# Kernel optimization log

Measured on AMD Instinct MI355X. Metric: run time of the kernel, lower is better.

Reference implementation:

```python
import jax, jax.numpy as jnp
import numpy as np
from jax import lax

DIM = 256
MOTION = 128
HEADS = 8
HID = int(DIM * 3.0)
EPS = 1e-5


def std_ln(x, w, b):
    # standard nn.LayerNorm: biased var, /sqrt(var+eps)
    mean = x.mean(-1, keepdims=True)
    var = jnp.var(x, axis=-1, keepdims=True)
    return w * (x - mean) / jnp.sqrt(var + EPS) + b


def custom_ln(x, w, b):
    # repo's custom LayerNorm: UNBIASED std (ddof=1) and divide by (std+eps)
    mean = x.mean(-1, keepdims=True)
    std = jnp.std(x, axis=-1, ddof=1, keepdims=True)
    return w * (x - mean) / (std + EPS) + b


def setup_inputs() -> dict:
    key = jax.random.key(0)
    ks = jax.random.split(key, 32)
    s = 0.02
    d = {}
    d['x'] = jax.random.normal(ks[0], (4, 16384, DIM), jnp.float32)
    d['cor'] = jax.random.uniform(ks[1], (4, 128, 128, 2), jnp.float32)
    # attention projections (qkv_bias=False)
    d['q_w'] = jax.random.normal(ks[2], (DIM, DIM), jnp.float32) * s
    d['kv_w'] = jax.random.normal(ks[3], (2 * DIM, DIM), jnp.float32) * s
    d['cor_w'] = jax.random.normal(ks[4], (MOTION, 2), jnp.float32) * s
    hd = DIM // HEADS
    md = MOTION // HEADS
    d['kln_w'] = jnp.ones((HEADS, 1, hd), jnp.float32)
    d['kln_b'] = jnp.zeros((HEADS, 1, hd), jnp.float32)
    d['vln_w'] = jnp.ones((HEADS, 1, hd), jnp.float32)
    d['vln_b'] = jnp.zeros((HEADS, 1, hd), jnp.float32)
    d['corln_w'] = jnp.ones((HEADS, 1, md), jnp.float32)
    d['corln_b'] = jnp.zeros((HEADS, 1, md), jnp.float32)
    d['op1_w'] = jax.random.normal(ks[5], (DIM, DIM), jnp.float32) * s
    d['op1_b'] = jnp.zeros((DIM,), jnp.float32)
    d['op2_w'] = jax.random.normal(ks[6], (DIM, DIM), jnp.float32) * s
    d['op2_b'] = jnp.zeros((DIM,), jnp.float32)
    d['om1_w'] = jax.random.normal(ks[7], (MOTION, MOTION), jnp.float32) * s
    d['om1_b'] = jnp.zeros((MOTION,), jnp.float32)
    d['om2_w'] = jax.random.normal(ks[8], (MOTION, MOTION), jnp.float32) * s
    d['om2_b'] = jnp.zeros((MOTION,), jnp.float32)
    d['norm1_w'] = jnp.ones((DIM,), jnp.float32)
    d['norm1_b'] = jnp.zeros((DIM,), jnp.float32)
    d['norm2_w'] = jnp.ones((DIM,), jnp.float32)
    d['norm2_b'] = jnp.zeros((DIM,), jnp.float32)
    d['fc1_w'] = jax.random.normal(ks[9], (HID, DIM), jnp.float32) * s
    d['fc1_b'] = jnp.zeros((HID,), jnp.float32)
    d['dw_w'] = jax.random.normal(ks[10], (HID, 1, 3, 3), jnp.float32) * np.sqrt(2.0 / 9.0)
    d['dw_b'] = jnp.zeros((HID,), jnp.float32)
    d['fc2_w'] = jax.random.normal(ks[11], (DIM, HID), jnp.float32) * s
    d['fc2_b'] = jnp.zeros((DIM,), jnp.float32)
    d['H'] = 128
    d['W'] = 128
    d['B'] = 2
    return d


def _forward(x, cor, q_w, kv_w, cor_w, kln_w, kln_b, vln_w, vln_b,
             corln_w, corln_b, op1_w, op1_b, op2_w, op2_b,
             om1_w, om1_b, om2_w, om2_b, norm1_w, norm1_b,
             norm2_w, norm2_b, fc1_w, fc1_b, dw_w, dw_b, fc2_w, fc2_b,
             H, W, B):
    gelu = lambda t: jax.nn.gelu(t, approximate=False)
    nwB = 2 * B
    N = H * W
    C = x.shape[-1]
    M = cor_w.shape[0]
    h = kln_w.shape[0]
    hd = C // h
    md = M // h
    hid = fc1_w.shape[0]

    xw = x.reshape(nwB, N, C)            # window_partition with full window == identity
    corw = cor.reshape(nwB, N, 2)

    xn = std_ln(xw, norm1_w, norm1_b)
    half = nwB // 2
    xr = jnp.concatenate([xn[half:], xn[:half]], axis=0)  # swap frame halves

    q = (xn @ q_w.T).reshape(nwB, N, h, hd).transpose(0, 2, 1, 3)          # bhnd
    kv = (xr @ kv_w.T).reshape(nwB, N, 2, h, hd)
    k = kv[:, :, 0].transpose(0, 2, 1, 3)
    v = kv[:, :, 1].transpose(0, 2, 1, 3)
    ce_flat = corw @ cor_w.T                                               # (nwB,N,M)
    ce = ce_flat.reshape(nwB, N, h, md).transpose(0, 2, 1, 3)

    k = custom_ln(k, kln_w, kln_b)
    v = custom_ln(v, vln_w, vln_b)
    ce = custom_ln(ce, corln_w, corln_b)

    # linear attention: (k^T v)/N then q @ .
    ktv = jnp.einsum('bhnd,bhne->bhde', k, v) / N
    app = jnp.einsum('bhnd,bhde->bhne', q, ktv).transpose(0, 2, 1, 3).reshape(nwB, N, C)
    t = app + xn                                   # shortcut bias = x_norm
    x_app = gelu(t @ op1_w.T + op1_b) @ op2_w.T + op2_b + xn

    ktc = jnp.einsum('bhnd,bhne->bhde', k, ce) / N
    crev = jnp.einsum('bhnd,bhde->bhne', q, ktc).transpose(0, 2, 1, 3).reshape(nwB, N, M)
    dm = crev - ce_flat
    motion = gelu(dm @ om1_w.T + om1_b) @ om2_w.T + om2_b

    x_back = xn + x_app

    # Mlp with depthwise conv
    y = std_ln(x_back, norm2_w, norm2_b)
    h1 = y @ fc1_w.T + fc1_b                       # (nwB,N,hid)
    img = h1.transpose(0, 2, 1).reshape(nwB, hid, H, W)
    conv = lax.conv_general_dilated(img, dw_w, (1, 1), 'SAME',
                                    feature_group_count=hid,
                                    dimension_numbers=('NCHW', 'OIHW', 'NCHW'))
    conv = conv + dw_b[None, :, None, None]
    h2 = gelu(conv.reshape(nwB, hid, N).transpose(0, 2, 1))
    out = h2 @ fc2_w.T + fc2_b

    x_out = xw + out
    return x_out, motion


def reference(x, cor, q_w, kv_w, cor_w, kln_w, kln_b, vln_w, vln_b,
              corln_w, corln_b, op1_w, op1_b, op2_w, op2_b,
              om1_w, om1_b, om2_w, om2_b, norm1_w, norm1_b,
              norm2_w, norm2_b, fc1_w, fc1_b, dw_w, dw_b, fc2_w, fc2_b,
              H, W, B):
    return _forward(x, cor, q_w, kv_w, cor_w, kln_w, kln_b, vln_w, vln_b,
                    corln_w, corln_b, op1_w, op1_b, op2_w, op2_b,
                    om1_w, om1_b, om2_w, om2_b, norm1_w, norm1_b,
                    norm2_w, norm2_b, fc1_w, fc1_b, dw_w, dw_b, fc2_w, fc2_b,
                    H, W, B)
```

## Files before the change

### kernel.cpp

```cpp
#include <hip/hip_runtime.h>
#include <hip/hip_bf16.h>

#define NTOK 65536

typedef __attribute__((ext_vector_type(4))) float f32x4;
typedef __attribute__((ext_vector_type(8))) short bf16x8;

__device__ __forceinline__ float gelu_f(float x){
    float z = -2.30234438f * fmaf(0.044715f * x * x, x, x);
    float e = exp2f(z);
    return x * __builtin_amdgcn_rcpf(1.0f + e);
}
__device__ __forceinline__ float bf2f(unsigned short u){
    union { unsigned int i; float f; } w; w.i = ((unsigned int)u) << 16; return w.f;
}
__device__ __forceinline__ unsigned short f2bf(float f){
    __hip_bfloat16 h = __float2bfloat16(f);
    return *reinterpret_cast<unsigned short*>(&h);
}

__global__ __launch_bounds__(256) void wconv_kernel(const float* __restrict__ q_w, const float* __restrict__ kv_w,
                                                    const float* __restrict__ op1_w, const float* __restrict__ op2_w,
                                                    const float* __restrict__ om1_w, const float* __restrict__ om2_w,
                                                    const float* __restrict__ fc1_w, const float* __restrict__ fc2_w,
                                                    unsigned short* __restrict__ Wb){
    size_t e = ((size_t)blockIdx.x * 256 + threadIdx.x) * 4;
    if (e >= 753664) return;
    const float* src; size_t off;
    if      (e <  65536){ src = q_w;   off = 0; }
    else if (e < 196608){ src = kv_w;  off = 65536; }
    else if (e < 262144){ src = op1_w; off = 196608; }
    else if (e < 327680){ src = op2_w; off = 262144; }
    else if (e < 344064){ src = om1_w; off = 327680; }
    else if (e < 360448){ src = om2_w; off = 344064; }
    else if (e < 557056){ src = fc1_w; off = 360448; }
    else                { src = fc2_w; off = 557056; }
    float4 v = *reinterpret_cast<const float4*>(src + (e - off));
    ushort4 o; o.x = f2bf(v.x); o.y = f2bf(v.y); o.z = f2bf(v.z); o.w = f2bf(v.w);
    *reinterpret_cast<ushort4*>(Wb + e) = o;
}

template<bool BF16IN>
__global__ __launch_bounds__(256) void stdln_kernel(const void* __restrict__ Xp,
                                                    const float* __restrict__ w,
                                                    const float* __restrict__ b,
                                                    unsigned short* __restrict__ out){
    int wv = threadIdx.x >> 6, lane = threadIdx.x & 63;
    int tok0 = (blockIdx.x * 4 + wv) * 8;
    int c0 = lane * 4;
    float4 w4 = *reinterpret_cast<const float4*>(w + c0);
    float4 b4 = *reinterpret_cast<const float4*>(b + c0);
    #pragma unroll 2
    for (int j = 0; j < 8; j++){
        size_t base = (size_t)(tok0 + j) * 256 + c0;
        float v[4];
        if constexpr (BF16IN){
            ushort4 u = *reinterpret_cast<const ushort4*>((const unsigned short*)Xp + base);
            v[0] = bf2f(u.x); v[1] = bf2f(u.y); v[2] = bf2f(u.z); v[3] = bf2f(u.w);
        } else {
            float4 f = *reinterpret_cast<const float4*>((const float*)Xp + base);
            v[0] = f.x; v[1] = f.y; v[2] = f.z; v[3] = f.w;
        }
        float s = v[0] + v[1] + v[2] + v[3];
        #pragma unroll
        for (int m = 1; m < 64; m <<= 1) s += __shfl_xor(s, m, 64);
        float mean = s * (1.0f / 256.0f);
        float ss = 0;
        #pragma unroll
        for (int k = 0; k < 4; k++){ v[k] -= mean; ss = fmaf(v[k], v[k], ss); }
        #pragma unroll
        for (int m = 1; m < 64; m <<= 1) ss += __shfl_xor(ss, m, 64);
        float inv = rsqrtf(ss * (1.0f / 256.0f) + 1e-5f);
        ushort4 o;
        o.x = f2bf(w4.x * v[0] * inv + b4.x);
        o.y = f2bf(w4.y * v[1] * inv + b4.y);
        o.z = f2bf(w4.z * v[2] * inv + b4.z);
        o.w = f2bf(w4.w * v[3] * inv + b4.w);
        *reinterpret_cast<ushort4*>(out + base) = o;
    }
}

__global__ __launch_bounds__(256) void ce_kernel(const float* __restrict__ cor,
                                                 const float* __restrict__ cor_w,
                                                 unsigned short* __restrict__ CEF){
    int m = threadIdx.x & 127, half = threadIdx.x >> 7;
    float w0 = cor_w[m * 2 + 0], w1 = cor_w[m * 2 + 1];
    #pragma unroll 4
    for (int it = 0; it < 16; it++){
        int tok = blockIdx.x * 32 + it * 2 + half;
        float c0 = cor[(size_t)tok * 2 + 0];
        float c1 = cor[(size_t)tok * 2 + 1];
        CEF[(size_t)tok * 128 + m] = f2bf(c0 * w0 + c1 * w1);
    }
}

__global__ __launch_bounds__(256) void ktvc_kernel(const unsigned short* __restrict__ Kb,
                                                   const unsigned short* __restrict__ Vb,
                                                   const unsigned short* __restrict__ CEF,
                                                   const float* __restrict__ kw, const float* __restrict__ kbb,
                                                   const float* __restrict__ vw, const float* __restrict__ vbb,
                                                   const float* __restrict__ cw, const float* __restrict__ cbb,
                                                   float* __restrict__ KTV, float* __restrict__ KTC){
    int bh = blockIdx.x, b = bh >> 3, h = bh & 7;
    __shared__ float Ks[64][36];
    __shared__ float Vs[64][36];
    __shared__ float Cs[64][20];
    __shared__ float P[2][64][24];
    int t = threadIdx.x;
    int lr = t >> 2, lq = t & 3;
    int g = t >> 6, tl = t & 63;
    int d0 = (tl >> 3) * 4, e0 = (tl & 7) * 4, e0c = (tl & 7) * 2;
    float kwr[8], kbr[8], vwr[8], vbr[8], cwr[4], cbr[4];
    #pragma unroll
    for (int j = 0; j < 8; j++){
        kwr[j] = kw[h * 32 + lq * 8 + j]; kbr[j] = kbb[h * 32 + lq * 8 + j];
        vwr[j] = vw[h * 32 + lq * 8 + j]; vbr[j] = vbb[h * 32 + lq * 8 + j];
    }
    #pragma unroll
    for (int j = 0; j < 4; j++){
        cwr[j] = cw[h * 16 + lq * 4 + j]; cbr[j] = cbb[h * 16 + lq * 4 + j];
    }
    float akv[4][4] = {};
    float akc[4][2] = {};
    size_t base = ((size_t)b << 14) + (size_t)blockIdx.y * 512;
    for (int n0 = 0; n0 < 512; n0 += 64){
        size_t rowi = base + n0 + lr;
        const ushort4* kp = reinterpret_cast<const ushort4*>(Kb + rowi * 256 + h * 32 + lq * 8);
        ushort4 ka = kp[0], kc = kp[1];
        const ushort4* vp = reinterpret_cast<const ushort4*>(Vb + rowi * 256 + h * 32 + lq * 8);
        ushort4 va = vp[0], vc = vp[1];
        ushort4 ca = *reinterpret_cast<const ushort4*>(CEF + rowi * 128 + h * 16 + lq * 4);
        float kvv[8] = { bf2f(ka.x), bf2f(ka.y), bf2f(ka.z), bf2f(ka.w),
                         bf2f(kc.x), bf2f(kc.y), bf2f(kc.z), bf2f(kc.w) };
        float vvv[8] = { bf2f(va.x), bf2f(va.y), bf2f(va.z), bf2f(va.w),
                         bf2f(vc.x), bf2f(vc.y), bf2f(vc.z), bf2f(vc.w) };
        float cvv[4] = { bf2f(ca.x), bf2f(ca.y), bf2f(ca.z), bf2f(ca.w) };
        float s = 0;
        #pragma unroll
        for (int j = 0; j < 8; j++) s += kvv[j];
        s += __shfl_xor(s, 1, 64); s += __shfl_xor(s, 2, 64);
        float mean = s * (1.0f / 32.0f);
        float ss = 0;
        #pragma unroll
        for (int j = 0; j < 8; j++){ kvv[j] -= mean; ss = fmaf(kvv[j], kvv[j], ss); }
        ss += __shfl_xor(ss, 1, 64); ss += __shfl_xor(ss, 2, 64);
        float inv = 1.0f / (sqrtf(ss * (1.0f / 31.0f)) + 1e-5f);
        #pragma unroll
        for (int j = 0; j < 8; j++) kvv[j] = fmaf(kwr[j] * kvv[j], inv, kbr[j]);
        s = 0;
        #pragma unroll
        for (int j = 0; j < 8; j++) s += vvv[j];
        s += __shfl_xor(s, 1, 64); s += __shfl_xor(s, 2, 64);
        mean = s * (1.0f / 32.0f);
        ss = 0;
        #pragma unroll
        for (int j = 0; j < 8; j++){ vvv[j] -= mean; ss = fmaf(vvv[j], vvv[j], ss); }
        ss += __shfl_xor(ss, 1, 64); ss += __shfl_xor(ss, 2, 64);
        inv = 1.0f / (sqrtf(ss * (1.0f / 31.0f)) + 1e-5f);
        #pragma unroll
        for (int j = 0; j < 8; j++) vvv[j] = fmaf(vwr[j] * vvv[j], inv, vbr[j]);
        s = 0;
        #pragma unroll
        for (int j = 0; j < 4; j++) s += cvv[j];
        s += __shfl_xor(s, 1, 64); s += __shfl_xor(s, 2, 64);
        mean = s * (1.0f / 16.0f);
        ss = 0;
        #pragma unroll
        for (int j = 0; j < 4; j++){ cvv[j] -= mean; ss = fmaf(cvv[j], cvv[j], ss); }
        ss += __shfl_xor(ss, 1, 64); ss += __shfl_xor(ss, 2, 64);
        inv = 1.0f / (sqrtf(ss * (1.0f / 15.0f)) + 1e-5f);
        #pragma unroll
        for (int j = 0; j < 4; j++) cvv[j] = fmaf(cwr[j] * cvv[j], inv, cbr[j]);
        __syncthreads();
        #pragma unroll
        for (int j = 0; j < 8; j++){ Ks[lr][lq * 8 + j] = kvv[j]; Vs[lr][lq * 8 + j] = vvv[j]; }
        #pragma unroll
        for (int j = 0; j < 4; j++) Cs[lr][lq * 4 + j] = cvv[j];
        __syncthreads();
        #pragma unroll 4
        for (int i = 0; i < 16; i++){
            int n = g * 16 + i;
            float4 k4 = *reinterpret_cast<const float4*>(&Ks[n][d0]);
            float4 v4 = *reinterpret_cast<const float4*>(&Vs[n][e0]);
            float2 c2 = *reinterpret_cast<const float2*>(&Cs[n][e0c]);
            float kk[4] = { k4.x, k4.y, k4.z, k4.w };
            float vv[4] = { v4.x, v4.y, v4.z, v4.w };
            #pragma unroll
            for (int a = 0; a < 4; a++){
                akv[a][0] = fmaf(kk[a], vv[0], akv[a][0]);
                akv[a][1] = fmaf(kk[a], vv[1], akv[a][1]);
                akv[a][2] = fmaf(kk[a], vv[2], akv[a][2]);
                akv[a][3] = fmaf(kk[a], vv[3], akv[a][3]);
                akc[a][0] = fmaf(kk[a], c2.x, akc[a][0]);
                akc[a][1] = fmaf(kk[a], c2.y, akc[a][1]);
            }
        }
    }
    __syncthreads();
    if (g >= 2){
        float* p = &P[g - 2][tl][0];
        #pragma unroll
        for (int a = 0; a < 4; a++){
            #pragma unroll
            for (int e = 0; e < 4; e++) p[a * 4 + e] = akv[a][e];
            p[16 + a * 2 + 0] = akc[a][0];
            p[16 + a * 2 + 1] = akc[a][1];
        }
    }
    __syncthreads();
    if (g < 2){
        const float* p = &P[g][tl][0];
        #pragma unroll
        for (int a = 0; a < 4; a++){
            #pragma unroll
            for (int e = 0; e < 4; e++) akv[a][e] += p[a * 4 + e];
            akc[a][0] += p[16 + a * 2 + 0];
            akc[a][1] += p[16 + a * 2 + 1];
        }
    }
    __syncthreads();
    if (g == 1){
        float* p = &P[0][tl][0];
        #pragma unroll
        for (int a = 0; a < 4; a++){
            #pragma unroll
            for (int e = 0; e < 4; e++) p[a * 4 + e] = akv[a][e];
            p[16 + a * 2 + 0] = akc[a][0];
            p[16 + a * 2 + 1] = akc[a][1];
        }
    }
    __syncthreads();
    if (g == 0){
        const float* p = &P[0][tl][0];
        const float sc = 1.0f / 16384.0f;
        float* o = KTV + (size_t)bh * 1024;
        float* o2 = KTC + (size_t)bh * 512;
        #pragma unroll
        for (int a = 0; a < 4; a++){
            #pragma unroll
            for (int e = 0; e < 4; e++)
                atomicAdd(&o[(d0 + a) * 32 + e0 + e], (akv[a][e] + p[a * 4 + e]) * sc);
            atomicAdd(&o2[(d0 + a) * 16 + e0c + 0], (akc[a][0] + p[16 + a * 2 + 0]) * sc);
            atomicAdd(&o2[(d0 + a) * 16 + e0c + 1], (akc[a][1] + p[16 + a * 2 + 1]) * sc);
        }
    }
}

__global__ __launch_bounds__(256) void wcomb_kernel(const float* __restrict__ q_w,
                                                    const float* __restrict__ KTV,
                                                    const float* __restrict__ KTC,
                                                    unsigned short* __restrict__ WTC){
    int c = blockIdx.x;
    int b = blockIdx.y;
    int i = threadIdx.x;
    __shared__ float coef[32];
    int h = (c < 256) ? (c >> 5) : ((c - 256) >> 4);
    if (i < 32){
        if (c < 256) coef[i] = KTV[(size_t)((b * 8 + h) << 10) + i * 32 + (c & 31)];
        else         coef[i] = KTC[(size_t)((b * 8 + h) << 9)  + i * 16 + ((c - 256) & 15)];
    }
    __syncthreads();
    float acc = 0;
    #pragma unroll
    for (int d = 0; d < 32; d++) acc = fmaf(q_w[(size_t)(h * 32 + d) * 256 + i], coef[d], acc);
    WTC[((size_t)b * 384 + c) * 256 + i] = f2bf(acc);
}

__global__ __launch_bounds__(192) void dwconv_kernel(const unsigned short* __restrict__ H1,
                                                     const float* __restrict__ dww,
                                                     const float* __restrict__ dwb,
                                                     unsigned short* __restrict__ H2){
    int blk = blockIdx.x;
    int xq = blk & 3;
    int yb = (blk >> 2) & 31;
    int bb = blk >> 7;
    int y0 = yb * 4, x0 = xq * 32;
    int ch = threadIdx.x * 4;
    float w[9][4];
    #pragma unroll
    for (int k = 0; k < 9; k++)
        #pragma unroll
        for (int j = 0; j < 4; j++) w[k][j] = dww[(ch + j) * 9 + k];
    float bias[4] = { dwb[ch], dwb[ch+1], dwb[ch+2], dwb[ch+3] };
    size_t rb[6]; bool rv[6];
    #pragma unroll
    for (int r = 0; r < 6; r++){
        int yr = y0 - 1 + r;
        rv[r] = ((unsigned)yr <= 127u);
        int yc = yr < 0 ? 0 : (yr > 127 ? 127 : yr);
        rb[r] = ((size_t)((bb << 14) + (yc << 7))) * 768 + ch;
    }
    size_t ob[4];
    #pragma unroll
    for (int j = 0; j < 4; j++) ob[j] = ((size_t)((bb << 14) + ((y0 + j) << 7))) * 768 + ch;

    ushort4 cA[6], cB[6], cC[6], cD[6];
    const ushort4 Z = {0, 0, 0, 0};
    #define LOADR(DST, XX) do {                                               \
        int _x = (XX);                                                        \
        bool xv = ((unsigned)_x <= 127u);                                     \
        _Pragma("unroll")                                                     \
        for (int r = 0; r < 6; r++)                                           \
            DST[r] = (xv && rv[r]) ? *reinterpret_cast<const ushort4*>(H1 + rb[r] + (size_t)_x * 768) : Z; \
    } while (0)

    #define EMITB(SA, SB, SC, XX) do {                                        \
        _Pragma("unroll")                                                     \
        for (int j = 0; j < 4; j++){                                          \
            float acc[4];                                                     \
            _Pragma("unroll")                                                 \
            for (int q = 0; q < 4; q++) acc[q] = bias[q];                     \
            _Pragma("unroll")                                                 \
            for (int rr2 = 0; rr2 < 3; rr2++){                                \
                int ri = j + rr2;                                             \
                float a0=bf2f(SA[ri].x),a1=bf2f(SA[ri].y),a2=bf2f(SA[ri].z),a3=bf2f(SA[ri].w); \
                float b0=bf2f(SB[ri].x),b1=bf2f(SB[ri].y),b2=bf2f(SB[ri].z),b3=bf2f(SB[ri].w); \
                float c0=bf2f(SC[ri].x),c1=bf2f(SC[ri].y),c2=bf2f(SC[ri].z),c3=bf2f(SC[ri].w); \
                acc[0]=fmaf(a0,w[rr2*3+0][0],acc[0]); acc[0]=fmaf(b0,w[rr2*3+1][0],acc[0]); acc[0]=fmaf(c0,w[rr2*3+2][0],acc[0]); \
                acc[1]=fmaf(a1,w[rr2*3+0][1],acc[1]); acc[1]=fmaf(b1,w[rr2*3+1][1],acc[1]); acc[1]=fmaf(c1,w[rr2*3+2][1],acc[1]); \
                acc[2]=fmaf(a2,w[rr2*3+0][2],acc[2]); acc[2]=fmaf(b2,w[rr2*3+1][2],acc[2]); acc[2]=fmaf(c2,w[rr2*3+2][2],acc[2]); \
                acc[3]=fmaf(a3,w[rr2*3+0][3],acc[3]); acc[3]=fmaf(b3,w[rr2*3+1][3],acc[3]); acc[3]=fmaf(c3,w[rr2*3+2][3],acc[3]); \
            }                                                                 \
            ushort4 o;                                                        \
            o.x = f2bf(gelu_f(acc[0])); o.y = f2bf(gelu_f(acc[1]));           \
            o.z = f2bf(gelu_f(acc[2])); o.w = f2bf(gelu_f(acc[3]));           \
            *reinterpret_cast<ushort4*>(H2 + ob[j] + (size_t)(XX) * 768) = o; \
        }                                                                     \
    } while (0)

    LOADR(cD, x0 - 1);
    LOADR(cA, x0);
    LOADR(cB, x0 + 1);
    LOADR(cC, x0 + 2);
    #pragma unroll 1
    for (int g = 0; g < 8; g++){
        int x = x0 + g * 4;
        EMITB(cD, cA, cB, x);     LOADR(cD, x + 3);
        EMITB(cA, cB, cC, x + 1); LOADR(cA, x + 4);
        EMITB(cB, cC, cD, x + 2); LOADR(cB, x + 5);
        EMITB(cC, cD, cA, x + 3); LOADR(cC, x + 6);
    }
    #undef LOADR
    #undef EMITB
}

#define M_KV        1
#define M_BIAS_GELU 2
#define M_BIAS_ADD2 3
#define M_BIAS      4
#define M_BIAS_BF16 5
#define M_BIAS_ADDX 6
#define M_ATTN      7

template<int MODE, bool SWAP, int K, int O, int WN>
__global__ __launch_bounds__(128 * WN) void mgemm(const unsigned short* __restrict__ A,
                                                  const unsigned short* __restrict__ Wp,
                                                  const float* __restrict__ bias,
                                                  const void* __restrict__ add,
                                                  void* __restrict__ out0,
                                                  void* __restrict__ out1){
    constexpr int WAVES = 2 * WN;
    constexpr int BN = 64 * WN;
    constexpr int CH = 8 + 4 * WN;
    constexpr int NT = K / 32;
    __shared__ __align__(16) unsigned short As[2][128 * 32];
    __shared__ __align__(16) unsigned short Bs[2][BN * 32];
    const int t = threadIdx.x;
    const int lane = t & 63, wid = t >> 6;
    const int wm = wid & 1, wn = wid >> 1;
    const int row0 = blockIdx.x * 128;
    const int colB = blockIdx.y * BN;
    const unsigned short* W = Wp;
    if constexpr (MODE == M_ATTN) W += (size_t)(row0 >> 14) * (384 * 256);
    f32x4 acc[4][4];
    #pragma unroll
    for (int i = 0; i < 4; i++)
        #pragma unroll
        for (int j = 0; j < 4; j++){ f32x4 z = {0.f, 0.f, 0.f, 0.f}; acc[i][j] = z; }

    const int lr = lane >> 2;
    const int ls = lane & 3;
    const int kq = lane >> 4;
    const int rr = lane & 15;

    auto STAGE = [&](int buf, int kb){
        #pragma unroll
        for (int c = wid; c < CH; c += WAVES){
            int r16 = (c < 8) ? c : (c - 8);
            int row = r16 * 16 + lr;
            int ko = ls ^ ((row >> 1) & 3);
            if (c < 8){
                int ga = row0 + row;
                if (SWAP) ga ^= 32768;
                __builtin_amdgcn_global_load_lds(
                    (const __attribute__((address_space(1))) unsigned int*)(A + (size_t)ga * K + kb + ko * 8),
                    (__attribute__((address_space(3))) unsigned int*)(As[buf] + r16 * 512),
                    16, 0, 0);
            } else {
                int gc = colB + row;
                __builtin_amdgcn_global_load_lds(
                    (const __attribute__((address_space(1))) unsigned int*)(W + (size_t)gc * K + kb + ko * 8),
                    (__attribute__((address_space(3))) unsigned int*)(Bs[buf] + r16 * 512),
                    16, 0, 0);
            }
        }
    };

    STAGE(0, 0);
    asm volatile("s_waitcnt vmcnt(0)" ::: "memory");
    __builtin_amdgcn_s_barrier();
    #pragma unroll 1
    for (int tt = 0; tt < NT; tt++){
        int cur = tt & 1;
        if (tt + 1 < NT) STAGE(cur ^ 1, (tt + 1) * 32);
        bf16x8 af[4], bfr[4];
        #pragma unroll
        for (int m = 0; m < 4; m++){
            int row = wm * 64 + m * 16 + rr;
            int s = kq ^ ((row >> 1) & 3);
            af[m] = *reinterpret_cast<const bf16x8*>(As[cur] + row * 32 + s * 8);
        }
        #pragma unroll
        for (int n = 0; n < 4; n++){
            int row = wn * 64 + n * 16 + rr;
            int s = kq ^ ((row >> 1) & 3);
            bfr[n] = *reinterpret_cast<const bf16x8*>(Bs[cur] + row * 32 + s * 8);
        }
        #pragma unroll
        for (int m = 0; m < 4; m++)
            #pragma unroll
            for (int n = 0; n < 4; n++)
                acc[m][n] = __builtin_amdgcn_mfma_f32_16x16x32_bf16(af[m], bfr[n], acc[m][n], 0, 0, 0);
        if (tt + 1 < NT){
            asm volatile("s_waitcnt vmcnt(0)" ::: "memory");
            __builtin_amdgcn_s_barrier();
        }
    }

    #pragma unroll
    for (int m = 0; m < 4; m++){
        #pragma unroll
        for (int n = 0; n < 4; n++){
            int col = colB + wn * 64 + n * 16 + rr;
            int rbase = row0 + wm * 64 + m * 16 + kq * 4;
            #pragma unroll
            for (int j = 0; j < 4; j++){
                int r = rbase + j;
                float v = acc[m][n][j];
                size_t o = (size_t)r * O + col;
                if constexpr (MODE == M_KV){
                    if (col < 256) ((unsigned short*)out0)[(size_t)r * 256 + col] = f2bf(v);
                    else           ((unsigned short*)out1)[(size_t)r * 256 + col - 256] = f2bf(v);
                } else if constexpr (MODE == M_BIAS_GELU){
                    ((unsigned short*)out0)[o] = f2bf(gelu_f(v + bias[col]));
                } else if constexpr (MODE == M_BIAS_ADD2){
                    ((unsigned short*)out0)[o] = f2bf(v + bias[col] + 2.0f * bf2f(((const unsigned short*)add)[o]));
                } else if constexpr (MODE == M_BIAS){
                    ((float*)out0)[o] = v + bias[col];
                } else if constexpr (MODE == M_BIAS_BF16){
                    ((unsigned short*)out0)[o] = f2bf(v + bias[col]);
                } else if constexpr (MODE == M_BIAS_ADDX){
                    ((float*)out0)[o] = v + bias[col] + ((const float*)add)[o];
                } else if constexpr (MODE == M_ATTN){
                    if (col < 256){
                        size_t o1 = (size_t)r * 256 + col;
                        ((unsigned short*)out0)[o1] = f2bf(v + bf2f(((const unsigned short*)add)[o1]));
                    } else {
                        size_t o2 = (size_t)r * 128 + (col - 256);
                        ((unsigned short*)out1)[o2] = f2bf(v - bf2f(((const unsigned short*)bias)[o2]));
                    }
                }
            }
        }
    }
}

extern "C" void kernel_launch(void* const* d_in, const int* in_sizes, int n_in,
                              void* d_out, int out_size, void* d_ws, size_t ws_size,
                              hipStream_t stream){
    const float* x     = (const float*)d_in[0];
    const float* cor   = (const float*)d_in[1];
    const float* q_w   = (const float*)d_in[2];
    const float* kv_w  = (const float*)d_in[3];
    const float* cor_w = (const float*)d_in[4];
    const float* kln_w = (const float*)d_in[5];
    const float* kln_b = (const float*)d_in[6];
    const float* vln_w = (const float*)d_in[7];
    const float* vln_b = (const float*)d_in[8];
    const float* corln_w = (const float*)d_in[9];
    const float* corln_b = (const float*)d_in[10];
    const float* op1_w = (const float*)d_in[11];
    const float* op1_b = (const float*)d_in[12];
    const float* op2_w = (const float*)d_in[13];
    const float* op2_b = (const float*)d_in[14];
    const float* om1_w = (const float*)d_in[15];
    const float* om1_b = (const float*)d_in[16];
    const float* om2_w = (const float*)d_in[17];
    const float* om2_b = (const float*)d_in[18];
    const float* n1_w  = (const float*)d_in[19];
    const float* n1_b  = (const float*)d_in[20];
    const float* n2_w  = (const float*)d_in[21];
    const float* n2_b  = (const float*)d_in[22];
    const float* fc1_w = (const float*)d_in[23];
    const float* fc1_b = (const float*)d_in[24];
    const float* dw_w  = (const float*)d_in[25];
    const float* dw_b  = (const float*)d_in[26];
    const float* fc2_w = (const float*)d_in[27];
    const float* fc2_b = (const float*)d_in[28];

    unsigned short* XN  = (unsigned short*)d_ws;
    unsigned short* Qb  = XN  + (size_t)NTOK * 256;
    unsigned short* Kb  = Qb  + (size_t)NTOK * 256;
    unsigned short* Vb  = Kb  + (size_t)NTOK * 256;
    unsigned short* CEF = Vb  + (size_t)NTOK * 256;
    unsigned short* CE  = CEF + (size_t)NTOK * 128;
    float* KTV = (float*)(CE + (size_t)NTOK * 128);
    float* KTC = KTV + 32768;
    unsigned short* WTC = (unsigned short*)(KTC + 16384);
    unsigned short* Wb  = WTC + 4 * 384 * 256;
    unsigned short* H2  = Wb + 753664;
    unsigned short* T1 = Vb;
    unsigned short* T2 = Kb;
    unsigned short* XB = Qb;
    unsigned short* Y  = Vb;
    unsigned short* TM = CE;
    unsigned short* MH = CEF;
    unsigned short* H1 = XN;
    float* xout = (float*)d_out;
    float* mout = xout + (size_t)NTOK * 256;

    unsigned short* w_kv  = Wb + 65536;
    unsigned short* w_op1 = Wb + 196608;
    unsigned short* w_op2 = Wb + 262144;
    unsigned short* w_om1 = Wb + 327680;
    unsigned short* w_om2 = Wb + 344064;
    unsigned short* w_fc1 = Wb + 360448;
    unsigned short* w_fc2 = Wb + 557056;

    wconv_kernel<<<736, 256, 0, stream>>>(q_w, kv_w, op1_w, op2_w, om1_w, om2_w, fc1_w, fc2_w, Wb);
    stdln_kernel<false><<<2048, 256, 0, stream>>>(x, n1_w, n1_b, XN);
    mgemm<M_KV, true, 256, 512, 4><<<dim3(512, 2), 512, 0, stream>>>(XN, w_kv, nullptr, nullptr, Kb, Vb);
    ce_kernel<<<2048, 256, 0, stream>>>(cor, cor_w, CEF);
    hipMemsetAsync(KTV, 0, (32768 + 16384) * sizeof(float), stream);
    ktvc_kernel<<<dim3(32, 32), 256, 0, stream>>>(Kb, Vb, CEF, kln_w, kln_b, vln_w, vln_b,
                                                  corln_w, corln_b, KTV, KTC);
    wcomb_kernel<<<dim3(384, 4), 256, 0, stream>>>(q_w, KTV, KTC, WTC);
    mgemm<M_ATTN, false, 256, 384, 6><<<dim3(512, 1), 768, 0, stream>>>(XN, WTC, (const float*)CEF, XN, T1, TM);
    mgemm<M_BIAS_GELU, false, 256, 256, 4><<<dim3(512, 1), 512, 0, stream>>>(T1, w_op1, op1_b, nullptr, T2, nullptr);
    mgemm<M_BIAS_ADD2, false, 256, 256, 4><<<dim3(512, 1), 512, 0, stream>>>(T2, w_op2, op2_b, XN, XB, nullptr);
    mgemm<M_BIAS_GELU, false, 128, 128, 2><<<dim3(512, 1), 256, 0, stream>>>(TM, w_om1, om1_b, nullptr, MH, nullptr);
    mgemm<M_BIAS, false, 128, 128, 2><<<dim3(512, 1), 256, 0, stream>>>(MH, w_om2, om2_b, nullptr, mout, nullptr);
    stdln_kernel<true><<<2048, 256, 0, stream>>>(XB, n2_w, n2_b, Y);
    mgemm<M_BIAS_BF16, false, 256, 768, 6><<<dim3(512, 2), 768, 0, stream>>>(Y, w_fc1, fc1_b, nullptr, H1, nullptr);
    dwconv_kernel<<<512, 192, 0, stream>>>(H1, dw_w, dw_b, H2);
    mgemm<M_BIAS_ADDX, false, 768, 256, 4><<<dim3(512, 1), 512, 0, stream>>>(H2, w_fc2, fc2_b, x, xout, nullptr);
}
```

Measured before the change: 424.2 us.

## Stage GEMM epilogue through LDS for vectorized coalesced stores; widen KV GEMM tile

The GEMM epilogue now writes each wave's accumulator fragment into a padded LDS scratch region and reads it back row-wise. Global loads and stores then happen in 16-byte vectors, including the residual and add operands, instead of scattered 2- or 4-byte scalar accesses. The KV projection GEMM launches with WN=8 (1024 threads, one block column) so each block covers all 512 output columns. The cost is an extra LDS round trip and a barrier per block. The rounding order of the bf16 adds changes slightly, since the GEMM result is rounded to bf16 before the residual is added.

```diff
diff --git a/kernel.cpp b/kernel.cpp
--- a/kernel.cpp
+++ b/kernel.cpp
@@ -17,6 +17,13 @@
 __device__ __forceinline__ unsigned short f2bf(float f){
     __hip_bfloat16 h = __float2bfloat16(f);
     return *reinterpret_cast<unsigned short*>(&h);
+}
+__device__ __forceinline__ bf16x8 add_bf8(bf16x8 s, bf16x8 o, float k){
+    bf16x8 r;
+    #pragma unroll
+    for (int i = 0; i < 8; i++)
+        r[i] = (short)f2bf(fmaf(k, bf2f((unsigned short)o[i]), bf2f((unsigned short)s[i])));
+    return r;
 }
 
 __global__ __launch_bounds__(256) void wconv_kernel(const float* __restrict__ q_w, const float* __restrict__ kv_w,
@@ -363,8 +370,10 @@
     constexpr int BN = 64 * WN;
     constexpr int CH = 8 + 4 * WN;
     constexpr int NT = K / 32;
-    __shared__ __align__(16) unsigned short As[2][128 * 32];
-    __shared__ __align__(16) unsigned short Bs[2][BN * 32];
+    constexpr bool F32OUT = (MODE == M_BIAS || MODE == M_BIAS_ADDX);
+    __shared__ __align__(16) unsigned short SMEM[2 * 128 * 32 + 2 * BN * 32];
+    unsigned short* As0 = SMEM;
+    unsigned short* Bs0 = SMEM + 2 * 128 * 32;
     const int t = threadIdx.x;
     const int lane = t & 63, wid = t >> 6;
     const int wm = wid & 1, wn = wid >> 1;
@@ -394,13 +403,13 @@
                 if (SWAP) ga ^= 32768;
                 __builtin_amdgcn_global_load_lds(
                     (const __attribute__((address_space(1))) unsigned int*)(A + (size_t)ga * K + kb + ko * 8),
-                    (__attribute__((address_space(3))) unsigned int*)(As[buf] + r16 * 512),
+                    (__attribute__((address_space(3))) unsigned int*)(As0 + buf * 4096 + r16 * 512),
                     16, 0, 0);
             } else {
                 int gc = colB + row;
                 __builtin_amdgcn_global_load_lds(
                     (const __attribute__((address_space(1))) unsigned int*)(W + (size_t)gc * K + kb + ko * 8),
-                    (__attribute__((address_space(3))) unsigned int*)(Bs[buf] + r16 * 512),
+                    (__attribute__((address_space(3))) unsigned int*)(Bs0 + buf * (BN * 32) + r16 * 512),
                     16, 0, 0);
             }
         }
@@ -418,13 +427,13 @@
         for (int m = 0; m < 4; m++){
             int row = wm * 64 + m * 16 + rr;
             int s = kq ^ ((row >> 1) & 3);
-            af[m] = *reinterpret_cast<const bf16x8*>(As[cur] + row * 32 + s * 8);
+            af[m] = *reinterpret_cast<const bf16x8*>(As0 + cur * 4096 + row * 32 + s * 8);
         }
         #pragma unroll
         for (int n = 0; n < 4; n++){
             int row = wn * 64 + n * 16 + rr;
             int s = kq ^ ((row >> 1) & 3);
-            bfr[n] = *reinterpret_cast<const bf16x8*>(Bs[cur] + row * 32 + s * 8);
+            bfr[n] = *reinterpret_cast<const bf16x8*>(Bs0 + cur * (BN * 32) + row * 32 + s * 8);
         }
         #pragma unroll
         for (int m = 0; m < 4; m++)
@@ -437,38 +446,68 @@
         }
     }
 
+    __syncthreads();
+    unsigned short* scr = SMEM + (size_t)wid * 2304;
+    float* scrf = (float*)scr;
+    const int rloc = lane >> 2;
+    const int cs = (lane & 3) * 16;
     #pragma unroll
     for (int m = 0; m < 4; m++){
         #pragma unroll
         for (int n = 0; n < 4; n++){
             int col = colB + wn * 64 + n * 16 + rr;
-            int rbase = row0 + wm * 64 + m * 16 + kq * 4;
             #pragma unroll
             for (int j = 0; j < 4; j++){
-                int r = rbase + j;
                 float v = acc[m][n][j];
-                size_t o = (size_t)r * O + col;
+                int si = (kq * 4 + j) * 68 + n * 16 + rr;
+                if constexpr (MODE == M_KV)            scr[si] = f2bf(v);
+                else if constexpr (MODE == M_BIAS_GELU) scr[si] = f2bf(gelu_f(v + bias[col]));
+                else if constexpr (MODE == M_BIAS_ADD2) scr[si] = f2bf(v + bias[col]);
+                else if constexpr (MODE == M_BIAS_BF16) scr[si] = f2bf(v + bias[col]);
+                else if constexpr (MODE == M_ATTN)      scr[si] = f2bf(v);
+                else if constexpr (MODE == M_BIAS)      scrf[si] = v + bias[col];
+                else if constexpr (MODE == M_BIAS_ADDX) scrf[si] = v + bias[col];
+            }
+        }
+        int r = row0 + wm * 64 + m * 16 + rloc;
+        int colb = colB + wn * 64 + cs;
+        if constexpr (F32OUT){
+            #pragma unroll
+            for (int q = 0; q < 4; q++){
+                float4 vv = *reinterpret_cast<const float4*>(&scrf[rloc * 68 + cs + q * 4]);
+                size_t o = (size_t)r * O + colb + q * 4;
+                if constexpr (MODE == M_BIAS_ADDX){
+                    float4 xa = *reinterpret_cast<const float4*>(&((const float*)add)[o]);
+                    vv.x += xa.x; vv.y += xa.y; vv.z += xa.z; vv.w += xa.w;
+                }
+                *reinterpret_cast<float4*>(&((float*)out0)[o]) = vv;
+            }
+        } else {
+            #pragma unroll
+            for (int q = 0; q < 2; q++){
+                bf16x8 sv = *reinterpret_cast<const bf16x8*>(&scr[rloc * 68 + cs + q * 8]);
+                int cg = colb + q * 8;
                 if constexpr (MODE == M_KV){
-                    if (col < 256) ((unsigned short*)out0)[(size_t)r * 256 + col] = f2bf(v);
-                    else           ((unsigned short*)out1)[(size_t)r * 256 + col - 256] = f2bf(v);
-                } else if constexpr (MODE == M_BIAS_GELU){
-                    ((unsigned short*)out0)[o] = f2bf(gelu_f(v + bias[col]));
+                    unsigned short* dst = (cg < 256)
+                        ? (unsigned short*)out0 + (size_t)r * 256 + cg
+                        : (unsigned short*)out1 + (size_t)r * 256 + (cg - 256);
+                    *reinterpret_cast<bf16x8*>(dst) = sv;
+                } else if constexpr (MODE == M_ATTN){
+                    if (cg < 256){
+                        size_t o1 = (size_t)r * 256 + cg;
+                        bf16x8 xv = *reinterpret_cast<const bf16x8*>((const unsigned short*)add + o1);
+                        *reinterpret_cast<bf16x8*>((unsigned short*)out0 + o1) = add_bf8(sv, xv, 1.0f);
+                    } else {
+                        size_t o2 = (size_t)r * 128 + (cg - 256);
+                        bf16x8 cv = *reinterpret_cast<const bf16x8*>((const unsigned short*)bias + o2);
+                        *reinterpret_cast<bf16x8*>((unsigned short*)out1 + o2) = add_bf8(sv, cv, -1.0f);
+                    }
                 } else if constexpr (MODE == M_BIAS_ADD2){
-                    ((unsigned short*)out0)[o] = f2bf(v + bias[col] + 2.0f * bf2f(((const unsigned short*)add)[o]));
-                } else if constexpr (MODE == M_BIAS){
-                    ((float*)out0)[o] = v + bias[col];
-                } else if constexpr (MODE == M_BIAS_BF16){
-                    ((unsigned short*)out0)[o] = f2bf(v + bias[col]);
-                } else if constexpr (MODE == M_BIAS_ADDX){
-                    ((float*)out0)[o] = v + bias[col] + ((const float*)add)[o];
-                } else if constexpr (MODE == M_ATTN){
-                    if (col < 256){
-                        size_t o1 = (size_t)r * 256 + col;
-                        ((unsigned short*)out0)[o1] = f2bf(v + bf2f(((const unsigned short*)add)[o1]));
-                    } else {
-                        size_t o2 = (size_t)r * 128 + (col - 256);
-                        ((unsigned short*)out1)[o2] = f2bf(v - bf2f(((const unsigned short*)bias)[o2]));
-                    }
+                    size_t o = (size_t)r * O + cg;
+                    bf16x8 xv = *reinterpret_cast<const bf16x8*>((const unsigned short*)add + o);
+                    *reinterpret_cast<bf16x8*>((unsigned short*)out0 + o) = add_bf8(sv, xv, 2.0f);
+                } else {
+                    *reinterpret_cast<bf16x8*>((unsigned short*)out0 + (size_t)r * O + cg) = sv;
                 }
             }
         }
@@ -539,7 +578,7 @@
 
     wconv_kernel<<<736, 256, 0, stream>>>(q_w, kv_w, op1_w, op2_w, om1_w, om2_w, fc1_w, fc2_w, Wb);
     stdln_kernel<false><<<2048, 256, 0, stream>>>(x, n1_w, n1_b, XN);
-    mgemm<M_KV, true, 256, 512, 4><<<dim3(512, 2), 512, 0, stream>>>(XN, w_kv, nullptr, nullptr, Kb, Vb);
+    mgemm<M_KV, true, 256, 512, 8><<<dim3(512, 1), 1024, 0, stream>>>(XN, w_kv, nullptr, nullptr, Kb, Vb);
     ce_kernel<<<2048, 256, 0, stream>>>(cor, cor_w, CEF);
     hipMemsetAsync(KTV, 0, (32768 + 16384) * sizeof(float), stream);
     ktvc_kernel<<<dim3(32, 32), 256, 0, stream>>>(Kb, Vb, CEF, kln_w, kln_b, vln_w, vln_b,
```

New measurement: 413.4 us. 1.03x faster.
